# Kernel tuning notes

Hardware: AMD Instinct MI355X
Metric: run time of the kernel (lower is better)

Reference implementation:

```python
import jax, jax.numpy as jnp
import numpy as np

B, C, H, W = 8, 768, 32, 32
NH = 12
HD = C // NH
HID = 4 * C
EPS = 1e-5


def _layer_norm(x, g, b):
    mu = jnp.mean(x, axis=-1, keepdims=True)
    var = jnp.mean(jnp.square(x - mu), axis=-1, keepdims=True)
    return (x - mu) * jax.lax.rsqrt(var + EPS) * g + b


def setup_inputs() -> dict:
    key = jax.random.key(0)
    ks = jax.random.split(key, 12)
    s = 0.02
    return {
        "x": jax.random.normal(ks[0], (B, C, H, W), jnp.float32),
        "conv_w": jax.random.normal(ks[1], (C, 1, 3, 3), jnp.float32) * s,  # depthwise OIHW
        "conv_b": jnp.zeros((C,), jnp.float32),
        "ln1_g": jnp.ones((C,), jnp.float32),
        "ln1_b": jnp.zeros((C,), jnp.float32),
        "qkv_w": jax.random.normal(ks[2], (3 * C, C), jnp.float32) * s,  # no bias (qkv_bias=False)
        "proj_w": jax.random.normal(ks[3], (C, C), jnp.float32) * s,
        "proj_b": jnp.zeros((C,), jnp.float32),
        "ln2_g": jnp.ones((C,), jnp.float32),
        "ln2_b": jnp.zeros((C,), jnp.float32),
        "fc1_w": jax.random.normal(ks[4], (HID, C), jnp.float32) * s,
        "fc1_b": jnp.zeros((HID,), jnp.float32),
        "fc2_w": jax.random.normal(ks[5], (C, HID), jnp.float32) * s,
        "fc2_b": jnp.zeros((C,), jnp.float32),
    }


def reference(x, conv_w, conv_b, ln1_g, ln1_b, qkv_w, proj_w, proj_b,
              ln2_g, ln2_b, fc1_w, fc1_b, fc2_w, fc2_b):
    # depthwise 3x3 conv positional embedding, residual
    pe = jax.lax.conv_general_dilated(
        x, conv_w, window_strides=(1, 1), padding=((1, 1), (1, 1)),
        dimension_numbers=("NCHW", "OIHW", "NCHW"), feature_group_count=C)
    x = x + pe + conv_b[None, :, None, None]

    b, c, h, w = x.shape
    t = x.reshape(b, c, h * w).transpose(0, 2, 1)  # [B, N, C]

    # attention
    hn = _layer_norm(t, ln1_g, ln1_b)
    qkv = hn @ qkv_w.T  # [B, N, 3C]
    qkv = qkv.reshape(b, h * w, 3, NH, HD).transpose(2, 0, 3, 1, 4)  # [3, B, nh, N, hd]
    q, k, v = qkv[0], qkv[1], qkv[2]
    scale = HD ** -0.5
    attn = jax.nn.softmax(jnp.einsum("bhnd,bhmd->bhnm", q, k) * scale, axis=-1)
    o = jnp.einsum("bhnm,bhmd->bhnd", attn, v).transpose(0, 2, 1, 3).reshape(b, h * w, c)
    t = t + (o @ proj_w.T + proj_b)

    # MLP
    hn = _layer_norm(t, ln2_g, ln2_b)
    hid = jax.nn.gelu(hn @ fc1_w.T + fc1_b, approximate=False)
    t = t + (hid @ fc2_w.T + fc2_b)

    return t.transpose(0, 2, 1).reshape(b, c, h, w)
```

## Files before the change

kernel.cpp:

```cpp
#include <hip/hip_runtime.h>
#include <math.h>


typedef __bf16 bf16;
typedef __attribute__((ext_vector_type(8))) __bf16 bf16x8;
typedef __attribute__((ext_vector_type(4))) __bf16 bf16x4;
typedef __attribute__((ext_vector_type(4))) float f32x4;

#define B_   8
#define C_   768
#define N_   1024
#define NH_  12
#define HD_  64
#define HID_ 3072
#define NTOK   (B_ * N_)
#define NHEADS (B_ * NH_)
#define FA_C   0.1803368801111601f

__device__ __forceinline__ void gload_lds16(const void* g, void* l) {
  __builtin_amdgcn_global_load_lds(
      (__attribute__((address_space(1))) void*)(void*)g,
      (__attribute__((address_space(3))) void*)l, 16, 0, 0);
}

__device__ __forceinline__ float gelu1(float x) {
  float u = 0.7978845608028654f * x * (1.0f + 0.044715f * x * x);
  float e = __builtin_amdgcn_exp2f(u * 2.885390081777927f);
  float th = 1.0f - 2.0f * __builtin_amdgcn_rcpf(e + 1.0f);
  return 0.5f * x * (1.0f + th);
}

template <int BN, int EPI, bool REMAP>
__global__ __launch_bounds__(256) void gemm_bt(
    const bf16* __restrict__ A, const bf16* __restrict__ B, int K, int lda,
    int ldb, int ntiles, bf16* __restrict__ o0, bf16* __restrict__ o1,
    bf16* __restrict__ o2, float* __restrict__ resid,
    const float* __restrict__ bias, float* __restrict__ outp) {
  constexpr int JJ = BN / 32;
  constexpr int BCH = BN / 32;
  constexpr int STAGE_B = (128 + BN) * 64 * 2;
  constexpr int EXTRA_B = (EPI == 5) ? 64 * 132 * 4 : (EPI == 0 ? 128 * 256 : 0);
  constexpr int SMEM_B = STAGE_B > EXTRA_B ? STAGE_B : EXTRA_B;
  __shared__ __align__(16) char smemraw[SMEM_B];
  bf16* As = (bf16*)smemraw;
  bf16* Bs = As + 128 * 64;

  const int tid = threadIdx.x;
  const int wave = tid >> 6, lane = tid & 63;
  const int wm = wave & 1, wn = wave >> 1;
  const int lr = lane & 15, kq = lane >> 4;
  const int sw = lr & 7;

  int m0, n0;
  if constexpr (REMAP) {
    const int bid = blockIdx.x;
    const int g = bid & 7, s = bid >> 3;
    const int ms = s / ntiles;
    m0 = (g * 8 + ms) * 128;
    n0 = (s - ms * ntiles) * BN;
  } else {
    m0 = blockIdx.y * 128;
    n0 = blockIdx.x * BN;
  }

  f32x4 acc[4][JJ];
#pragma unroll
  for (int i = 0; i < 4; i++)
#pragma unroll
    for (int j = 0; j < JJ; j++) acc[i][j] = (f32x4){0.f, 0.f, 0.f, 0.f};

  const bf16* ap[4];
  const bf16* bp[BCH];
  {
    const bf16* Arow = A + (size_t)m0 * lda;
    const bf16* Brow = B + (size_t)n0 * ldb;
#pragma unroll
    for (int it = 0; it < 4; ++it) {
      int s = it * 256 + tid;
      int r = s >> 3, seg = (s & 7) ^ (r & 7);
      ap[it] = Arow + (size_t)r * lda + seg * 8;
    }
#pragma unroll
    for (int it = 0; it < BCH; ++it) {
      int s = it * 256 + tid;
      int r = s >> 3, seg = (s & 7) ^ (r & 7);
      bp[it] = Brow + (size_t)r * ldb + seg * 8;
    }
  }

  for (int k0 = 0; k0 < K; k0 += 64) {
#pragma unroll
    for (int it = 0; it < 4; ++it) {
      gload_lds16(ap[it], (char*)As + (it * 256 + tid) * 16);
      ap[it] += 64;
    }
#pragma unroll
    for (int it = 0; it < BCH; ++it) {
      gload_lds16(bp[it], (char*)Bs + (it * 256 + tid) * 16);
      bp[it] += 64;
    }
    __syncthreads();

#pragma unroll
    for (int h = 0; h < 2; ++h) {
      bf16x8 af[4], bfr[JJ];
      const int c = h * 4 + kq;
#pragma unroll
      for (int i = 0; i < 4; i++) {
        int row = wm * 64 + i * 16 + lr;
        af[i] = *(const bf16x8*)((char*)As + (row * 8 + (c ^ sw)) * 16);
      }
#pragma unroll
      for (int j = 0; j < JJ; j++) {
        int row = wn * (BN / 2) + j * 16 + lr;
        bfr[j] = *(const bf16x8*)((char*)Bs + (row * 8 + (c ^ sw)) * 16);
      }
#pragma unroll
      for (int i = 0; i < 4; i++)
#pragma unroll
        for (int j = 0; j < JJ; j++)
          acc[i][j] = __builtin_amdgcn_mfma_f32_16x16x32_bf16(bfr[j], af[i],
                                                              acc[i][j], 0, 0, 0);
    }
    __syncthreads();
  }

  if constexpr (EPI == 0) {
    const int b = m0 >> 10, tok0 = m0 & (N_ - 1);
    if (n0 < 2 * C_) {
      const int s = n0 >= C_ ? 1 : 0;
      bf16* dst = s ? o1 : o0;
#pragma unroll
      for (int i = 0; i < 4; i++) {
        const int m = m0 + wm * 64 + i * 16 + lr;
#pragma unroll
        for (int j = 0; j < JJ; j++) {
          const int rem = n0 - s * C_ + wn * (BN / 2) + j * 16 + kq * 4;
          const int h = rem >> 6, d = rem & 63;
          const f32x4 v = acc[i][j];
          bf16x4 pk = {(bf16)v[0], (bf16)v[1], (bf16)v[2], (bf16)v[3]};
          size_t head = (size_t)b * NH_ + h;
          *(bf16x4*)(dst + (head * N_ + (m & (N_ - 1))) * HD_ + d) = pk;
        }
      }
    } else {
      bf16* tile = (bf16*)smemraw;
#pragma unroll
      for (int i = 0; i < 4; i++) {
        const int ml = wm * 64 + i * 16 + lr;
        const int mc = ml >> 3, mo = ml & 7;
#pragma unroll
        for (int j = 0; j < JJ; j++) {
          const f32x4 v = acc[i][j];
#pragma unroll
          for (int r = 0; r < 4; r++) {
            const int nl = wn * (BN / 2) + j * 16 + kq * 4 + r;
            *(bf16*)((char*)tile + nl * 256 + ((mc ^ (nl & 15)) * 16) + mo * 2) =
                (bf16)v[r];
          }
        }
      }
      __syncthreads();
      const int nl = tid >> 1, mh = (tid & 1) * 64;
      const int vb = n0 - 2 * C_ + nl;
      const size_t head = (size_t)b * NH_ + (vb >> 6);
      bf16* dst = o2 + (head * HD_ + (vb & 63)) * N_ + tok0 + mh;
#pragma unroll
      for (int c8 = 0; c8 < 8; ++c8) {
        const int c = (mh >> 3) + c8;
        bf16x8 val = *(const bf16x8*)((char*)tile + nl * 256 +
                                      ((c ^ (nl & 15)) * 16));
        *(bf16x8*)(dst + c8 * 8) = val;
      }
    }
  } else if constexpr (EPI == 3) {
#pragma unroll
    for (int j = 0; j < JJ; j++) {
      const int n = n0 + wn * (BN / 2) + j * 16 + kq * 4;
      const f32x4 bv = *(const f32x4*)(bias + n);
#pragma unroll
      for (int i = 0; i < 4; i++) {
        const int m = m0 + wm * 64 + i * 16 + lr;
        float* rp = resid + (size_t)m * C_ + n;
        f32x4 old = *(const f32x4*)rp;
        const f32x4 v = acc[i][j];
        f32x4 nw = {old[0] + v[0] + bv[0], old[1] + v[1] + bv[1],
                    old[2] + v[2] + bv[2], old[3] + v[3] + bv[3]};
        *(f32x4*)rp = nw;
      }
    }
  } else if constexpr (EPI == 4) {
#pragma unroll
    for (int j = 0; j < JJ; j++) {
      const int n = n0 + wn * (BN / 2) + j * 16 + kq * 4;
      const f32x4 bv = *(const f32x4*)(bias + n);
#pragma unroll
      for (int i = 0; i < 4; i++) {
        const int m = m0 + wm * 64 + i * 16 + lr;
        const f32x4 v = acc[i][j];
        bf16x4 pk = {(bf16)gelu1(v[0] + bv[0]), (bf16)gelu1(v[1] + bv[1]),
                     (bf16)gelu1(v[2] + bv[2]), (bf16)gelu1(v[3] + bv[3])};
        *(bf16x4*)(o0 + (size_t)m * HID_ + n) = pk;
      }
    }
  } else if constexpr (EPI == 5) {
    float* tile = (float*)smemraw;
    const int b = m0 >> 10, tok0 = m0 & (N_ - 1);
#pragma unroll
    for (int j = 0; j < JJ; j++) {
      const int nl0 = wn * (BN / 2) + j * 16 + kq * 4;
      const int n = n0 + nl0;
      const f32x4 bv = *(const f32x4*)(bias + n);
#pragma unroll
      for (int i = 0; i < 4; i++) {
        const int ml = wm * 64 + i * 16 + lr;
        const float* rp = resid + (size_t)(m0 + ml) * C_ + n;
        f32x4 old = *(const f32x4*)rp;
        const f32x4 v = acc[i][j];
#pragma unroll
        for (int r = 0; r < 4; r++)
          tile[(nl0 + r) * 132 + ml] = old[r] + v[r] + bv[r];
      }
    }
    __syncthreads();
    const int nl = tid & 63, mc = tid >> 6;
    float* dst = outp + ((size_t)(b * C_ + n0 + nl)) * N_ + tok0 + mc * 32;
    const float* src = tile + nl * 132 + mc * 32;
#pragma unroll
    for (int q = 0; q < 8; ++q)
      *(f32x4*)(dst + q * 4) = *(const f32x4*)(src + q * 4);
  }
}

__global__ __launch_bounds__(256, 3) void flash_attn(
    const bf16* __restrict__ Qb, const bf16* __restrict__ Kb,
    const bf16* __restrict__ Vt, bf16* __restrict__ attn) {
  __shared__ __align__(16) bf16 ksm[2][64 * 64];
  __shared__ __align__(16) bf16 vsm[2][64 * 64];
  __shared__ __align__(16) bf16 psm[4][32 * 64];

  const int tid = threadIdx.x, wave = tid >> 6, lane = tid & 63;
  const int lr = lane & 15, kq = lane >> 4;
  const int head = blockIdx.y;
  const int b = head / NH_, hh = head - b * NH_;
  const int q0 = blockIdx.x * 128;
  const bf16* Qh = Qb + (size_t)head * (N_ * HD_);
  const bf16* Kh = Kb + (size_t)head * (N_ * HD_);
  const bf16* Vh = Vt + (size_t)head * (HD_ * N_);
  char* pw = (char*)&psm[wave][0];

  bf16x8 qf[2][2];
#pragma unroll
  for (int j = 0; j < 2; ++j)
#pragma unroll
    for (int kh = 0; kh < 2; ++kh)
      qf[j][kh] = *(const bf16x8*)(Qh +
                                   (size_t)(q0 + wave * 32 + j * 16 + lr) * HD_ +
                                   kh * 32 + kq * 8);

  f32x4 o[4][2];
#pragma unroll
  for (int i = 0; i < 4; i++)
#pragma unroll
    for (int j = 0; j < 2; j++) o[i][j] = (f32x4){0.f, 0.f, 0.f, 0.f};
  float mprev[2] = {-1e30f, -1e30f}, lacc[2] = {0.f, 0.f};

  auto stage = [&](int t, int bi) {
#pragma unroll
    for (int it = 0; it < 2; ++it) {
      int s = it * 256 + tid;
      int r = s >> 3, seg = (s & 7) ^ (r & 7);
      gload_lds16(Kh + (size_t)(t * 64 + r) * HD_ + seg * 8,
                  (char*)ksm[bi] + (it * 256 + wave * 64) * 16);
    }
#pragma unroll
    for (int it = 0; it < 2; ++it) {
      int s = it * 256 + tid;
      int r = s >> 3, seg = (s & 7) ^ (r & 7);
      gload_lds16(Vh + (size_t)r * N_ + t * 64 + seg * 8,
                  (char*)vsm[bi] + (it * 256 + wave * 64) * 16);
    }
  };

  stage(0, 0);

  for (int t = 0; t < 16; ++t) {
    const int bi = t & 1;
    __syncthreads();
    if (t < 15) stage(t + 1, bi ^ 1);

    f32x4 sacc[4][2];
#pragma unroll
    for (int i = 0; i < 4; ++i) {
#pragma unroll
      for (int j = 0; j < 2; ++j) sacc[i][j] = (f32x4){0.f, 0.f, 0.f, 0.f};
      int row = i * 16 + lr;
      bf16x8 kf0 = *(const bf16x8*)((char*)ksm[bi] + row * 128 +
                                    ((kq ^ (row & 7)) * 16));
      bf16x8 kf1 = *(const bf16x8*)((char*)ksm[bi] + row * 128 +
                                    (((4 + kq) ^ (row & 7)) * 16));
#pragma unroll
      for (int j = 0; j < 2; ++j) {
        sacc[i][j] = __builtin_amdgcn_mfma_f32_16x16x32_bf16(kf0, qf[j][0],
                                                             sacc[i][j], 0, 0, 0);
        sacc[i][j] = __builtin_amdgcn_mfma_f32_16x16x32_bf16(kf1, qf[j][1],
                                                             sacc[i][j], 0, 0, 0);
      }
    }

#pragma unroll
    for (int j = 0; j < 2; ++j) {
      float mx = -1e30f;
#pragma unroll
      for (int i = 0; i < 4; ++i)
#pragma unroll
        for (int r = 0; r < 4; ++r) mx = fmaxf(mx, sacc[i][j][r]);
      mx = fmaxf(mx, __shfl_xor(mx, 16));
      mx = fmaxf(mx, __shfl_xor(mx, 32));
      float mnew = fmaxf(mprev[j], mx);
      float alpha = __builtin_amdgcn_exp2f((mprev[j] - mnew) * FA_C);
      mprev[j] = mnew;
      float rs = 0.f;
      const int prow = j * 16 + lr;
#pragma unroll
      for (int i = 0; i < 4; ++i) {
        float p0 = __builtin_amdgcn_exp2f((sacc[i][j][0] - mnew) * FA_C);
        float p1 = __builtin_amdgcn_exp2f((sacc[i][j][1] - mnew) * FA_C);
        float p2 = __builtin_amdgcn_exp2f((sacc[i][j][2] - mnew) * FA_C);
        float p3 = __builtin_amdgcn_exp2f((sacc[i][j][3] - mnew) * FA_C);
        rs += (p0 + p1) + (p2 + p3);
        bf16x4 pk = {(bf16)p0, (bf16)p1, (bf16)p2, (bf16)p3};
        int c = i * 2 + (kq >> 1);
        *(bf16x4*)(pw + prow * 128 + ((c ^ (prow & 7)) * 16) + (kq & 1) * 8) = pk;
      }
      rs += __shfl_xor(rs, 16);
      rs += __shfl_xor(rs, 32);
      lacc[j] = lacc[j] * alpha + rs;
#pragma unroll
      for (int i = 0; i < 4; ++i) {
        o[i][j][0] *= alpha; o[i][j][1] *= alpha;
        o[i][j][2] *= alpha; o[i][j][3] *= alpha;
      }
    }

#pragma unroll
    for (int k0c = 0; k0c < 2; ++k0c) {
      bf16x8 pf[2];
#pragma unroll
      for (int j = 0; j < 2; ++j) {
        int prow = j * 16 + lr, c = k0c * 4 + kq;
        pf[j] = *(const bf16x8*)(pw + prow * 128 + ((c ^ (prow & 7)) * 16));
      }
#pragma unroll
      for (int i = 0; i < 4; ++i) {
        int d = i * 16 + lr, c = k0c * 4 + kq;
        bf16x8 vf = *(const bf16x8*)((char*)vsm[bi] + d * 128 +
                                     ((c ^ (d & 7)) * 16));
#pragma unroll
        for (int j = 0; j < 2; ++j)
          o[i][j] = __builtin_amdgcn_mfma_f32_16x16x32_bf16(vf, pf[j], o[i][j],
                                                            0, 0, 0);
      }
    }
  }

#pragma unroll
  for (int j = 0; j < 2; ++j) {
    float inv = 1.0f / lacc[j];
    int tok = q0 + wave * 32 + j * 16 + lr;
    bf16* op = attn + ((size_t)(b * N_ + tok)) * C_ + hh * HD_;
#pragma unroll
    for (int i = 0; i < 4; ++i) {
      bf16x4 pk = {(bf16)(o[i][j][0] * inv), (bf16)(o[i][j][1] * inv),
                   (bf16)(o[i][j][2] * inv), (bf16)(o[i][j][3] * inv)};
      *(bf16x4*)(op + i * 16 + kq * 4) = pk;
    }
  }
}

__global__ __launch_bounds__(256) void cast_all(
    const float* __restrict__ a, int na, const float* __restrict__ b, int nb,
    const float* __restrict__ c, int nc, const float* __restrict__ d,
    bf16* __restrict__ dst) {
  int i = (blockIdx.x * 256 + threadIdx.x) * 4;
  const float* src;
  int off;
  if (i < na) { src = a; off = i; }
  else if (i < na + nb) { src = b; off = i - na; }
  else if (i < na + nb + nc) { src = c; off = i - na - nb; }
  else { src = d; off = i - na - nb - nc; }
  float4 v = *(const float4*)(src + off);
  bf16x4 o = {(bf16)v.x, (bf16)v.y, (bf16)v.z, (bf16)v.w};
  *(bf16x4*)(dst + i) = o;
}

__global__ __launch_bounds__(256) void conv_pe_t(const float* __restrict__ x,
                                                 const float* __restrict__ cw,
                                                 const float* __restrict__ cb,
                                                 float* __restrict__ t0) {
  __shared__ float tile[32][33];
  const int h = blockIdx.x, ct = blockIdx.y, b = blockIdx.z;
  const int tid = threadIdx.x;
  const int w = tid & 31, cs = tid >> 5;
#pragma unroll
  for (int cc = cs; cc < 32; cc += 8) {
    int c = ct * 32 + cc;
    const float* xp = x + ((size_t)(b * C_ + c)) * 1024;
    const float* wp = cw + c * 9;
    float s = cb[c] + xp[h * 32 + w];
#pragma unroll
    for (int ky = 0; ky < 3; ++ky) {
      int hy = h + ky - 1;
      if ((unsigned)hy < 32u) {
#pragma unroll
        for (int kx = 0; kx < 3; ++kx) {
          int wx = w + kx - 1;
          if ((unsigned)wx < 32u) s += xp[hy * 32 + wx] * wp[ky * 3 + kx];
        }
      }
    }
    tile[cc][w] = s;
  }
  __syncthreads();
  const int cc = tid & 31;
#pragma unroll
  for (int wc = tid >> 5; wc < 32; wc += 8)
    t0[((size_t)(b * N_) + h * 32 + wc) * C_ + ct * 32 + cc] = tile[cc][wc];
}

__global__ __launch_bounds__(256) void ln_bf16(const float* __restrict__ t,
                                               const float* __restrict__ g,
                                               const float* __restrict__ be,
                                               bf16* __restrict__ out) {
  int row = blockIdx.x, tid = threadIdx.x;
  const float* p = t + (size_t)row * C_;
  float v0 = p[tid], v1 = p[tid + 256], v2 = p[tid + 512];
  __shared__ float rs[256], rq[256];
  rs[tid] = v0 + v1 + v2;
  rq[tid] = v0 * v0 + v1 * v1 + v2 * v2;
  __syncthreads();
  for (int off = 128; off; off >>= 1) {
    if (tid < off) {
      rs[tid] += rs[tid + off];
      rq[tid] += rq[tid + off];
    }
    __syncthreads();
  }
  float mu = rs[0] * (1.f / C_);
  float var = rq[0] * (1.f / C_) - mu * mu;
  float rstd = rsqrtf(var + 1e-5f);
  bf16* q = out + (size_t)row * C_;
  q[tid] = (bf16)((v0 - mu) * rstd * g[tid] + be[tid]);
  q[tid + 256] = (bf16)((v1 - mu) * rstd * g[tid + 256] + be[tid + 256]);
  q[tid + 512] = (bf16)((v2 - mu) * rstd * g[tid + 512] + be[tid + 512]);
}

extern "C" void kernel_launch(void* const* d_in, const int* in_sizes, int n_in,
                              void* d_out, int out_size, void* d_ws,
                              size_t ws_size, hipStream_t stream) {
  (void)in_sizes; (void)n_in; (void)out_size; (void)ws_size;
  const float* x      = (const float*)d_in[0];
  const float* conv_w = (const float*)d_in[1];
  const float* conv_b = (const float*)d_in[2];
  const float* ln1_g  = (const float*)d_in[3];
  const float* ln1_b  = (const float*)d_in[4];
  const float* qkv_w  = (const float*)d_in[5];
  const float* proj_w = (const float*)d_in[6];
  const float* proj_b = (const float*)d_in[7];
  const float* ln2_g  = (const float*)d_in[8];
  const float* ln2_b  = (const float*)d_in[9];
  const float* fc1_w  = (const float*)d_in[10];
  const float* fc1_b  = (const float*)d_in[11];
  const float* fc2_w  = (const float*)d_in[12];
  const float* fc2_b  = (const float*)d_in[13];
  float* out = (float*)d_out;

  char* w = (char*)d_ws;
  auto carve = [&](size_t bytes) {
    char* p = w;
    w += (bytes + 255) & ~(size_t)255;
    return p;
  };
  bf16* hid   = (bf16*)carve((size_t)NTOK * HID_ * 2);
  float* t0   = (float*)carve((size_t)NTOK * C_ * 4);
  bf16* lnout = (bf16*)carve((size_t)NTOK * C_ * 2);
  bf16* wq    = (bf16*)carve((size_t)3 * C_ * C_ * 2);
  bf16* wp    = (bf16*)carve((size_t)C_ * C_ * 2);
  bf16* w1    = (bf16*)carve((size_t)HID_ * C_ * 2);
  bf16* w2    = (bf16*)carve((size_t)C_ * HID_ * 2);
  bf16* Qb    = (bf16*)carve((size_t)NHEADS * N_ * HD_ * 2);
  bf16* Kb    = (bf16*)carve((size_t)NHEADS * N_ * HD_ * 2);
  bf16* Vt    = (bf16*)carve((size_t)NHEADS * HD_ * N_ * 2);
  bf16* attn  = (bf16*)carve((size_t)NTOK * C_ * 2);

  const int na = 3 * C_ * C_, nb = C_ * C_, nc = HID_ * C_, nd = C_ * HID_;
  cast_all<<<(na + nb + nc + nd) / 1024, 256, 0, stream>>>(
      qkv_w, na, proj_w, nb, fc1_w, nc, fc2_w, wq);

  conv_pe_t<<<dim3(32, C_ / 32, B_), 256, 0, stream>>>(x, conv_w, conv_b, t0);

  ln_bf16<<<NTOK, 256, 0, stream>>>(t0, ln1_g, ln1_b, lnout);
  gemm_bt<128, 0, true><<<1152, 256, 0, stream>>>(
      lnout, wq, 768, 768, 768, 18, Qb, Kb, Vt, nullptr, nullptr, nullptr);

  flash_attn<<<dim3(N_ / 128, NHEADS), 256, 0, stream>>>(Qb, Kb, Vt, attn);

  gemm_bt<64, 3, true><<<768, 256, 0, stream>>>(
      attn, wp, 768, 768, 768, 12, nullptr, nullptr, nullptr, t0, proj_b,
      nullptr);
  ln_bf16<<<NTOK, 256, 0, stream>>>(t0, ln2_g, ln2_b, lnout);
  gemm_bt<128, 4, true><<<1536, 256, 0, stream>>>(
      lnout, w1, 768, 768, 768, 24, hid, nullptr, nullptr, nullptr, fc1_b,
      nullptr);
  gemm_bt<64, 5, true><<<768, 256, 0, stream>>>(
      hid, w2, 3072, 3072, 3072, 12, nullptr, nullptr, nullptr, t0, fc2_b,
      out);
}
```

Measured before the change: 405.1 us.

## Add 256x256-tile 512-thread fc1 GEMM with quarter-staged LDS pipeline and fused GELU

Replaces the fc1 GEMM (128-wide tiles, 1536 blocks) with a new kernel using 256x256 output tiles, 8 waves and a double-buffered LDS of 128KB. Each k-step is split into four quadrant MFMA phases, with async global-to-LDS loads for the next stage issued between them and priority raised around the MFMA bursts. The goal is more data reuse per loaded byte and better overlap of loads with matrix math. In exchange it uses heavy LDS and registers, which limits occupancy to one block per CU, and launches 384 blocks, which may leave the 256 CUs unevenly loaded.

```diff
diff --git a/kernel.cpp b/kernel.cpp
--- a/kernel.cpp
+++ b/kernel.cpp
@@ -28,6 +28,238 @@
   float e = __builtin_amdgcn_exp2f(u * 2.885390081777927f);
   float th = 1.0f - 2.0f * __builtin_amdgcn_rcpf(e + 1.0f);
   return 0.5f * x * (1.0f + th);
+}
+
+#define PIPE_SYNC(N)                                              \
+  do {                                                            \
+    asm volatile("s_waitcnt vmcnt(" #N ") lgkmcnt(0)" ::: "memory"); \
+    __builtin_amdgcn_sched_barrier(0);                            \
+    __builtin_amdgcn_s_barrier();                                 \
+    __builtin_amdgcn_sched_barrier(0);                            \
+    asm volatile("" ::: "memory");                                \
+  } while (0)
+
+__global__ __launch_bounds__(512) void gemm256_gelu(
+    const bf16* __restrict__ A, const bf16* __restrict__ Bw,
+    const float* __restrict__ bias, bf16* __restrict__ outp,
+    int K, int lda, int ldb, int ntiles, int mtpx, int ldo) {
+  __shared__ __align__(16) char smem[131072];
+  const int tid = threadIdx.x;
+  const int wave = tid >> 6, lane = tid & 63;
+  const int wr = wave & 1, wc = wave >> 1;
+  const int lr = lane & 15, kq = lane >> 4;
+
+  const int bid = blockIdx.x;
+  const int g = bid & 7, s = bid >> 3;
+  const int ms = s / ntiles;
+  const int m0 = (g * mtpx + ms) * 256;
+  const int n0 = (s - ms * ntiles) * 256;
+
+  f32x4 acc[2][2][4][2];
+#pragma unroll
+  for (int qm = 0; qm < 2; ++qm)
+#pragma unroll
+    for (int qn = 0; qn < 2; ++qn)
+#pragma unroll
+      for (int i = 0; i < 4; ++i)
+#pragma unroll
+        for (int j = 0; j < 2; ++j)
+          acc[qm][qn][i][j] = (f32x4){0.f, 0.f, 0.f, 0.f};
+
+  const bf16* pa[2][2];
+  const bf16* pb[2][2];
+  int dof[2];
+#pragma unroll
+  for (int ld = 0; ld < 2; ++ld) {
+    const int sidx = ld * 512 + tid;
+    const int r = sidx >> 3, seg = (sidx & 7) ^ (r & 7);
+    pa[0][ld] = A + (size_t)(m0 + r) * lda + seg * 8;
+    pa[1][ld] = A + (size_t)(m0 + 128 + r) * lda + seg * 8;
+    pb[0][ld] = Bw + (size_t)(n0 + r) * ldb + seg * 8;
+    pb[1][ld] = Bw + (size_t)(n0 + 128 + r) * ldb + seg * 8;
+    dof[ld] = sidx * 16;
+  }
+
+  const int NT = K >> 6;
+
+  {
+    char* wb = smem;
+#pragma unroll
+    for (int ld = 0; ld < 2; ++ld) gload_lds16(pa[0][ld], wb + dof[ld]);
+#pragma unroll
+    for (int ld = 0; ld < 2; ++ld) gload_lds16(pb[0][ld], wb + 32768 + dof[ld]);
+#pragma unroll
+    for (int ld = 0; ld < 2; ++ld) gload_lds16(pa[1][ld], wb + 16384 + dof[ld]);
+#pragma unroll
+    for (int ld = 0; ld < 2; ++ld) gload_lds16(pb[1][ld], wb + 49152 + dof[ld]);
+#pragma unroll
+    for (int ld = 0; ld < 2; ++ld) {
+      pa[0][ld] += 64; pa[1][ld] += 64; pb[0][ld] += 64; pb[1][ld] += 64;
+    }
+  }
+
+  for (int t = 0; t < NT - 1; ++t) {
+    const char* rb = smem + (t & 1) * 65536;
+    char* wb = smem + ((t & 1) ^ 1) * 65536;
+    bf16x8 af0[4][2], af1[4][2], bf0[2][2], bf1[2][2];
+
+    PIPE_SYNC(4);
+#pragma unroll
+    for (int i = 0; i < 4; ++i) {
+      const int r = wr * 64 + i * 16 + lr;
+#pragma unroll
+      for (int kh = 0; kh < 2; ++kh) {
+        const int c = kh * 4 + kq;
+        af0[i][kh] = *(const bf16x8*)(rb + (r * 8 + (c ^ (r & 7))) * 16);
+      }
+    }
+#pragma unroll
+    for (int j = 0; j < 2; ++j) {
+      const int r = wc * 32 + j * 16 + lr;
+#pragma unroll
+      for (int kh = 0; kh < 2; ++kh) {
+        const int c = kh * 4 + kq;
+        bf0[j][kh] = *(const bf16x8*)(rb + 32768 + (r * 8 + (c ^ (r & 7))) * 16);
+      }
+    }
+    gload_lds16(pa[0][0], wb + dof[0]);
+    gload_lds16(pa[0][1], wb + dof[1]);
+    pa[0][0] += 64; pa[0][1] += 64;
+    __builtin_amdgcn_s_setprio(1);
+#pragma unroll
+    for (int kh = 0; kh < 2; ++kh)
+#pragma unroll
+      for (int i = 0; i < 4; ++i)
+#pragma unroll
+        for (int j = 0; j < 2; ++j)
+          acc[0][0][i][j] = __builtin_amdgcn_mfma_f32_16x16x32_bf16(
+              bf0[j][kh], af0[i][kh], acc[0][0][i][j], 0, 0, 0);
+    __builtin_amdgcn_s_setprio(0);
+
+    PIPE_SYNC(4);
+#pragma unroll
+    for (int i = 0; i < 4; ++i) {
+      const int r = wr * 64 + i * 16 + lr;
+#pragma unroll
+      for (int kh = 0; kh < 2; ++kh) {
+        const int c = kh * 4 + kq;
+        af1[i][kh] = *(const bf16x8*)(rb + 16384 + (r * 8 + (c ^ (r & 7))) * 16);
+      }
+    }
+    gload_lds16(pb[0][0], wb + 32768 + dof[0]);
+    gload_lds16(pb[0][1], wb + 32768 + dof[1]);
+    pb[0][0] += 64; pb[0][1] += 64;
+    __builtin_amdgcn_s_setprio(1);
+#pragma unroll
+    for (int kh = 0; kh < 2; ++kh)
+#pragma unroll
+      for (int i = 0; i < 4; ++i)
+#pragma unroll
+        for (int j = 0; j < 2; ++j)
+          acc[1][0][i][j] = __builtin_amdgcn_mfma_f32_16x16x32_bf16(
+              bf0[j][kh], af1[i][kh], acc[1][0][i][j], 0, 0, 0);
+    __builtin_amdgcn_s_setprio(0);
+
+    PIPE_SYNC(4);
+#pragma unroll
+    for (int j = 0; j < 2; ++j) {
+      const int r = wc * 32 + j * 16 + lr;
+#pragma unroll
+      for (int kh = 0; kh < 2; ++kh) {
+        const int c = kh * 4 + kq;
+        bf1[j][kh] = *(const bf16x8*)(rb + 49152 + (r * 8 + (c ^ (r & 7))) * 16);
+      }
+    }
+    gload_lds16(pa[1][0], wb + 16384 + dof[0]);
+    gload_lds16(pa[1][1], wb + 16384 + dof[1]);
+    pa[1][0] += 64; pa[1][1] += 64;
+    __builtin_amdgcn_s_setprio(1);
+#pragma unroll
+    for (int kh = 0; kh < 2; ++kh)
+#pragma unroll
+      for (int i = 0; i < 4; ++i)
+#pragma unroll
+        for (int j = 0; j < 2; ++j)
+          acc[0][1][i][j] = __builtin_amdgcn_mfma_f32_16x16x32_bf16(
+              bf1[j][kh], af0[i][kh], acc[0][1][i][j], 0, 0, 0);
+    __builtin_amdgcn_s_setprio(0);
+
+    PIPE_SYNC(4);
+    gload_lds16(pb[1][0], wb + 49152 + dof[0]);
+    gload_lds16(pb[1][1], wb + 49152 + dof[1]);
+    pb[1][0] += 64; pb[1][1] += 64;
+    __builtin_amdgcn_s_setprio(1);
+#pragma unroll
+    for (int kh = 0; kh < 2; ++kh)
+#pragma unroll
+      for (int i = 0; i < 4; ++i)
+#pragma unroll
+        for (int j = 0; j < 2; ++j)
+          acc[1][1][i][j] = __builtin_amdgcn_mfma_f32_16x16x32_bf16(
+              bf1[j][kh], af1[i][kh], acc[1][1][i][j], 0, 0, 0);
+    __builtin_amdgcn_s_setprio(0);
+  }
+
+  {
+    const char* rb = smem + ((NT - 1) & 1) * 65536;
+    bf16x8 af0[4][2], af1[4][2], bf0[2][2], bf1[2][2];
+    PIPE_SYNC(0);
+#pragma unroll
+    for (int i = 0; i < 4; ++i) {
+      const int r = wr * 64 + i * 16 + lr;
+#pragma unroll
+      for (int kh = 0; kh < 2; ++kh) {
+        const int c = kh * 4 + kq;
+        af0[i][kh] = *(const bf16x8*)(rb + (r * 8 + (c ^ (r & 7))) * 16);
+        af1[i][kh] = *(const bf16x8*)(rb + 16384 + (r * 8 + (c ^ (r & 7))) * 16);
+      }
+    }
+#pragma unroll
+    for (int j = 0; j < 2; ++j) {
+      const int r = wc * 32 + j * 16 + lr;
+#pragma unroll
+      for (int kh = 0; kh < 2; ++kh) {
+        const int c = kh * 4 + kq;
+        bf0[j][kh] = *(const bf16x8*)(rb + 32768 + (r * 8 + (c ^ (r & 7))) * 16);
+        bf1[j][kh] = *(const bf16x8*)(rb + 49152 + (r * 8 + (c ^ (r & 7))) * 16);
+      }
+    }
+    __builtin_amdgcn_s_setprio(1);
+#pragma unroll
+    for (int kh = 0; kh < 2; ++kh)
+#pragma unroll
+      for (int i = 0; i < 4; ++i)
+#pragma unroll
+        for (int j = 0; j < 2; ++j) {
+          acc[0][0][i][j] = __builtin_amdgcn_mfma_f32_16x16x32_bf16(
+              bf0[j][kh], af0[i][kh], acc[0][0][i][j], 0, 0, 0);
+          acc[1][0][i][j] = __builtin_amdgcn_mfma_f32_16x16x32_bf16(
+              bf0[j][kh], af1[i][kh], acc[1][0][i][j], 0, 0, 0);
+          acc[0][1][i][j] = __builtin_amdgcn_mfma_f32_16x16x32_bf16(
+              bf1[j][kh], af0[i][kh], acc[0][1][i][j], 0, 0, 0);
+          acc[1][1][i][j] = __builtin_amdgcn_mfma_f32_16x16x32_bf16(
+              bf1[j][kh], af1[i][kh], acc[1][1][i][j], 0, 0, 0);
+        }
+    __builtin_amdgcn_s_setprio(0);
+  }
+
+#pragma unroll
+  for (int qn = 0; qn < 2; ++qn)
+#pragma unroll
+    for (int j = 0; j < 2; ++j) {
+      const int n = n0 + qn * 128 + wc * 32 + j * 16 + kq * 4;
+      const f32x4 bv = *(const f32x4*)(bias + n);
+#pragma unroll
+      for (int qm = 0; qm < 2; ++qm)
+#pragma unroll
+        for (int i = 0; i < 4; ++i) {
+          const int m = m0 + qm * 128 + wr * 64 + i * 16 + lr;
+          const f32x4 v = acc[qm][qn][i][j];
+          bf16x4 pk = {(bf16)gelu1(v[0] + bv[0]), (bf16)gelu1(v[1] + bv[1]),
+                       (bf16)gelu1(v[2] + bv[2]), (bf16)gelu1(v[3] + bv[3])};
+          *(bf16x4*)(outp + (size_t)m * ldo + n) = pk;
+        }
+    }
 }
 
 template <int BN, int EPI, bool REMAP>
@@ -509,9 +741,8 @@
       attn, wp, 768, 768, 768, 12, nullptr, nullptr, nullptr, t0, proj_b,
       nullptr);
   ln_bf16<<<NTOK, 256, 0, stream>>>(t0, ln2_g, ln2_b, lnout);
-  gemm_bt<128, 4, true><<<1536, 256, 0, stream>>>(
-      lnout, w1, 768, 768, 768, 24, hid, nullptr, nullptr, nullptr, fc1_b,
-      nullptr);
+  gemm256_gelu<<<384, 512, 0, stream>>>(lnout, w1, fc1_b, hid, 768, 768, 768,
+                                        12, 4, HID_);
   gemm_bt<64, 5, true><<<768, 256, 0, stream>>>(
       hid, w2, 3072, 3072, 3072, 12, nullptr, nullptr, nullptr, t0, fc2_b,
       out);
```

New measurement: 403.2 us. About the same (-0.5%).

## Add dedicated 256x192-tile pipelined fc1 GEMM with fused GELU

Applied to the files above, without the earlier changes.

Replaces the generic 128x128 gemm_bt used for fc1 with a specialized 512-thread kernel using 256x192 output tiles, double-buffered LDS fed by direct global-to-LDS loads, and loads interleaved between MFMA phases with explicit waitcnt/barrier staging and setprio. Launch count drops to 512 blocks, one per CU-ish wave, with XCD-aware block remapping. Larger tiles raise arithmetic intensity and the staged pipeline aims to hide load latency, at the cost of higher register pressure (96 accumulator vectors) and 112KB LDS limiting occupancy to one block per CU.

```diff
diff --git a/kernel.cpp b/kernel.cpp
--- a/kernel.cpp
+++ b/kernel.cpp
@@ -28,6 +28,206 @@
   float e = __builtin_amdgcn_exp2f(u * 2.885390081777927f);
   float th = 1.0f - 2.0f * __builtin_amdgcn_rcpf(e + 1.0f);
   return 0.5f * x * (1.0f + th);
+}
+
+#define PIPE_SYNC(N)                                              \
+  do {                                                            \
+    asm volatile("s_waitcnt vmcnt(" #N ") lgkmcnt(0)" ::: "memory"); \
+    __builtin_amdgcn_sched_barrier(0);                            \
+    __builtin_amdgcn_s_barrier();                                 \
+    __builtin_amdgcn_sched_barrier(0);                            \
+    asm volatile("" ::: "memory");                                \
+  } while (0)
+
+__global__ __launch_bounds__(512) void gemm_fc1(
+    const bf16* __restrict__ A, const bf16* __restrict__ Bw,
+    const float* __restrict__ bias, bf16* __restrict__ outp,
+    int K, int lda, int ldb, int ntiles, int mtpx, int ldo) {
+  __shared__ __align__(16) char smem[114688];
+  const int tid = threadIdx.x;
+  const int wave = tid >> 6, lane = tid & 63;
+  const int wr = wave & 1, wc = wave >> 1;
+  const int lr = lane & 15, kq = lane >> 4;
+
+  const int bid = blockIdx.x;
+  const int g = bid & 7, s = bid >> 3;
+  const int ms = s / ntiles;
+  const int m0 = (g * mtpx + ms) * 256;
+  const int n0 = (s - ms * ntiles) * 192;
+
+  f32x4 acc[8][3];
+#pragma unroll
+  for (int i = 0; i < 8; ++i)
+#pragma unroll
+    for (int j = 0; j < 3; ++j) acc[i][j] = (f32x4){0.f, 0.f, 0.f, 0.f};
+
+  const bf16* pa[4];
+  const bf16* pb[3];
+  int da[4], db[3];
+#pragma unroll
+  for (int c = 0; c < 4; ++c) {
+    const int sidx = c * 512 + tid;
+    const int r = sidx >> 3, seg = (sidx & 7) ^ (r & 7);
+    pa[c] = A + (size_t)(m0 + r) * lda + seg * 8;
+    da[c] = sidx * 16;
+  }
+#pragma unroll
+  for (int c = 0; c < 3; ++c) {
+    const int sidx = c * 512 + tid;
+    const int r = sidx >> 3, seg = (sidx & 7) ^ (r & 7);
+    pb[c] = Bw + (size_t)(n0 + r) * ldb + seg * 8;
+    db[c] = 32768 + sidx * 16;
+  }
+
+  const int NT = K >> 6;
+
+  gload_lds16(pb[0], smem + db[0]);
+  gload_lds16(pb[1], smem + db[1]);
+  gload_lds16(pb[2], smem + db[2]);
+  gload_lds16(pa[0], smem + da[0]);
+  gload_lds16(pa[1], smem + da[1]);
+  gload_lds16(pa[2], smem + da[2]);
+  gload_lds16(pa[3], smem + da[3]);
+#pragma unroll
+  for (int c = 0; c < 4; ++c) pa[c] += 64;
+#pragma unroll
+  for (int c = 0; c < 3; ++c) pb[c] += 64;
+
+  for (int t = 0; t < NT - 1; ++t) {
+    const char* rb = smem + (t & 1) * 57344;
+    char* wb = smem + ((t & 1) ^ 1) * 57344;
+    bf16x8 af[4], bf0[3], bf1[3];
+
+    PIPE_SYNC(1);
+#pragma unroll
+    for (int i = 0; i < 4; ++i) {
+      const int r = wr * 128 + i * 16 + lr;
+      af[i] = *(const bf16x8*)(rb + (r * 8 + (kq ^ (r & 7))) * 16);
+    }
+#pragma unroll
+    for (int j = 0; j < 3; ++j) {
+      const int r = wc * 48 + j * 16 + lr;
+      bf0[j] = *(const bf16x8*)(rb + 32768 + (r * 8 + (kq ^ (r & 7))) * 16);
+    }
+    gload_lds16(pb[0], wb + db[0]); pb[0] += 64;
+    gload_lds16(pb[1], wb + db[1]); pb[1] += 64;
+    __builtin_amdgcn_s_setprio(1);
+#pragma unroll
+    for (int i = 0; i < 4; ++i)
+#pragma unroll
+      for (int j = 0; j < 3; ++j)
+        acc[i][j] = __builtin_amdgcn_mfma_f32_16x16x32_bf16(bf0[j], af[i],
+                                                            acc[i][j], 0, 0, 0);
+    __builtin_amdgcn_s_setprio(0);
+
+    PIPE_SYNC(2);
+#pragma unroll
+    for (int i = 0; i < 4; ++i) {
+      const int r = wr * 128 + 64 + i * 16 + lr;
+      af[i] = *(const bf16x8*)(rb + (r * 8 + (kq ^ (r & 7))) * 16);
+    }
+    gload_lds16(pb[2], wb + db[2]); pb[2] += 64;
+    gload_lds16(pa[0], wb + da[0]); pa[0] += 64;
+    __builtin_amdgcn_s_setprio(1);
+#pragma unroll
+    for (int i = 0; i < 4; ++i)
+#pragma unroll
+      for (int j = 0; j < 3; ++j)
+        acc[4 + i][j] = __builtin_amdgcn_mfma_f32_16x16x32_bf16(
+            bf0[j], af[i], acc[4 + i][j], 0, 0, 0);
+    __builtin_amdgcn_s_setprio(0);
+
+    PIPE_SYNC(4);
+#pragma unroll
+    for (int i = 0; i < 4; ++i) {
+      const int r = wr * 128 + i * 16 + lr;
+      af[i] = *(const bf16x8*)(rb + (r * 8 + ((4 + kq) ^ (r & 7))) * 16);
+    }
+#pragma unroll
+    for (int j = 0; j < 3; ++j) {
+      const int r = wc * 48 + j * 16 + lr;
+      bf1[j] = *(const bf16x8*)(rb + 32768 + (r * 8 + ((4 + kq) ^ (r & 7))) * 16);
+    }
+    gload_lds16(pa[1], wb + da[1]); pa[1] += 64;
+    gload_lds16(pa[2], wb + da[2]); pa[2] += 64;
+    __builtin_amdgcn_s_setprio(1);
+#pragma unroll
+    for (int i = 0; i < 4; ++i)
+#pragma unroll
+      for (int j = 0; j < 3; ++j)
+        acc[i][j] = __builtin_amdgcn_mfma_f32_16x16x32_bf16(bf1[j], af[i],
+                                                            acc[i][j], 0, 0, 0);
+    __builtin_amdgcn_s_setprio(0);
+
+    PIPE_SYNC(6);
+#pragma unroll
+    for (int i = 0; i < 4; ++i) {
+      const int r = wr * 128 + 64 + i * 16 + lr;
+      af[i] = *(const bf16x8*)(rb + (r * 8 + ((4 + kq) ^ (r & 7))) * 16);
+    }
+    gload_lds16(pa[3], wb + da[3]); pa[3] += 64;
+    __builtin_amdgcn_s_setprio(1);
+#pragma unroll
+    for (int i = 0; i < 4; ++i)
+#pragma unroll
+      for (int j = 0; j < 3; ++j)
+        acc[4 + i][j] = __builtin_amdgcn_mfma_f32_16x16x32_bf16(
+            bf1[j], af[i], acc[4 + i][j], 0, 0, 0);
+    __builtin_amdgcn_s_setprio(0);
+  }
+
+  {
+    const char* rb = smem + ((NT - 1) & 1) * 57344;
+    bf16x8 af[4], bf0[3], bf1[3];
+    PIPE_SYNC(0);
+#pragma unroll
+    for (int j = 0; j < 3; ++j) {
+      const int r = wc * 48 + j * 16 + lr;
+      bf0[j] = *(const bf16x8*)(rb + 32768 + (r * 8 + (kq ^ (r & 7))) * 16);
+      bf1[j] = *(const bf16x8*)(rb + 32768 + (r * 8 + ((4 + kq) ^ (r & 7))) * 16);
+    }
+    __builtin_amdgcn_s_setprio(1);
+#pragma unroll
+    for (int half = 0; half < 2; ++half) {
+#pragma unroll
+      for (int i = 0; i < 4; ++i) {
+        const int r = wr * 128 + half * 64 + i * 16 + lr;
+        af[i] = *(const bf16x8*)(rb + (r * 8 + (kq ^ (r & 7))) * 16);
+      }
+#pragma unroll
+      for (int i = 0; i < 4; ++i)
+#pragma unroll
+        for (int j = 0; j < 3; ++j)
+          acc[half * 4 + i][j] = __builtin_amdgcn_mfma_f32_16x16x32_bf16(
+              bf0[j], af[i], acc[half * 4 + i][j], 0, 0, 0);
+#pragma unroll
+      for (int i = 0; i < 4; ++i) {
+        const int r = wr * 128 + half * 64 + i * 16 + lr;
+        af[i] = *(const bf16x8*)(rb + (r * 8 + ((4 + kq) ^ (r & 7))) * 16);
+      }
+#pragma unroll
+      for (int i = 0; i < 4; ++i)
+#pragma unroll
+        for (int j = 0; j < 3; ++j)
+          acc[half * 4 + i][j] = __builtin_amdgcn_mfma_f32_16x16x32_bf16(
+              bf1[j], af[i], acc[half * 4 + i][j], 0, 0, 0);
+    }
+    __builtin_amdgcn_s_setprio(0);
+  }
+
+#pragma unroll
+  for (int j = 0; j < 3; ++j) {
+    const int n = n0 + wc * 48 + j * 16 + kq * 4;
+    const f32x4 bv = *(const f32x4*)(bias + n);
+#pragma unroll
+    for (int i = 0; i < 8; ++i) {
+      const int m = m0 + wr * 128 + i * 16 + lr;
+      const f32x4 v = acc[i][j];
+      bf16x4 pk = {(bf16)gelu1(v[0] + bv[0]), (bf16)gelu1(v[1] + bv[1]),
+                   (bf16)gelu1(v[2] + bv[2]), (bf16)gelu1(v[3] + bv[3])};
+      *(bf16x4*)(outp + (size_t)m * ldo + n) = pk;
+    }
+  }
 }
 
 template <int BN, int EPI, bool REMAP>
@@ -187,20 +387,6 @@
         f32x4 nw = {old[0] + v[0] + bv[0], old[1] + v[1] + bv[1],
                     old[2] + v[2] + bv[2], old[3] + v[3] + bv[3]};
         *(f32x4*)rp = nw;
-      }
-    }
-  } else if constexpr (EPI == 4) {
-#pragma unroll
-    for (int j = 0; j < JJ; j++) {
-      const int n = n0 + wn * (BN / 2) + j * 16 + kq * 4;
-      const f32x4 bv = *(const f32x4*)(bias + n);
-#pragma unroll
-      for (int i = 0; i < 4; i++) {
-        const int m = m0 + wm * 64 + i * 16 + lr;
-        const f32x4 v = acc[i][j];
-        bf16x4 pk = {(bf16)gelu1(v[0] + bv[0]), (bf16)gelu1(v[1] + bv[1]),
-                     (bf16)gelu1(v[2] + bv[2]), (bf16)gelu1(v[3] + bv[3])};
-        *(bf16x4*)(o0 + (size_t)m * HID_ + n) = pk;
       }
     }
   } else if constexpr (EPI == 5) {
@@ -509,9 +695,8 @@
       attn, wp, 768, 768, 768, 12, nullptr, nullptr, nullptr, t0, proj_b,
       nullptr);
   ln_bf16<<<NTOK, 256, 0, stream>>>(t0, ln2_g, ln2_b, lnout);
-  gemm_bt<128, 4, true><<<1536, 256, 0, stream>>>(
-      lnout, w1, 768, 768, 768, 24, hid, nullptr, nullptr, nullptr, fc1_b,
-      nullptr);
+  gemm_fc1<<<512, 512, 0, stream>>>(lnout, w1, fc1_b, hid, 768, 768, 768,
+                                    16, 4, HID_);
   gemm_bt<64, 5, true><<<768, 256, 0, stream>>>(
       hid, w2, 3072, 3072, 3072, 12, nullptr, nullptr, nullptr, t0, fc2_b,
       out);
```

Result: faster. 385.7 us (-4.8%).

## Add dedicated 128x96-tile MLP GEMM kernel with explicit LDS pipeline sync

Applied to the files above, without the earlier changes.

Replaces the fc1 and fc2 GEMMs with a new kernel that uses 128x96 tiles, double-buffered direct-to-LDS loads with hand-placed waitcnt/barriers and setprio around MFMA bursts. It also uses launch bounds of 2 blocks per SM. The grid is remapped to 2048 and 512 blocks to balance tile counts across the 256 CUs and reduce wave quantization. The risk is a lower arithmetic intensity per tile and tighter register pressure.

```diff
diff --git a/kernel.cpp b/kernel.cpp
--- a/kernel.cpp
+++ b/kernel.cpp
@@ -30,6 +30,177 @@
   return 0.5f * x * (1.0f + th);
 }
 
+#define PIPE_SYNC(N)                                              \
+  do {                                                            \
+    asm volatile("s_waitcnt vmcnt(" #N ") lgkmcnt(0)" ::: "memory"); \
+    __builtin_amdgcn_sched_barrier(0);                            \
+    __builtin_amdgcn_s_barrier();                                 \
+    __builtin_amdgcn_sched_barrier(0);                            \
+    asm volatile("" ::: "memory");                                \
+  } while (0)
+
+#define TILE_END_SYNC()                                           \
+  do {                                                            \
+    asm volatile("s_waitcnt lgkmcnt(0)" ::: "memory");            \
+    __builtin_amdgcn_sched_barrier(0);                            \
+    __builtin_amdgcn_s_barrier();                                 \
+    __builtin_amdgcn_sched_barrier(0);                            \
+    asm volatile("" ::: "memory");                                \
+  } while (0)
+
+template <int EPI>
+__global__ __launch_bounds__(256, 2) void gemm_mlp(
+    const bf16* __restrict__ A, const bf16* __restrict__ Bw,
+    const float* __restrict__ bias, bf16* __restrict__ o_bf,
+    const float* __restrict__ resid, float* __restrict__ o_f32,
+    int K, int lda, int ldb, int ntiles, int mtpx, int ldo) {
+  __shared__ __align__(16) char smem[57344];
+  const int tid = threadIdx.x;
+  const int wave = tid >> 6, lane = tid & 63;
+  const int wr = wave & 1, wc = wave >> 1;
+  const int lr = lane & 15, kq = lane >> 4;
+
+  const int bid = blockIdx.x;
+  const int g = bid & 7, s = bid >> 3;
+  const int ms = s / ntiles;
+  const int m0 = (g * mtpx + ms) * 128;
+  const int n0 = (s - ms * ntiles) * 96;
+
+  f32x4 acc[4][3];
+#pragma unroll
+  for (int i = 0; i < 4; ++i)
+#pragma unroll
+    for (int j = 0; j < 3; ++j) acc[i][j] = (f32x4){0.f, 0.f, 0.f, 0.f};
+
+  const bf16* pa[4];
+  const bf16* pb[3];
+  int da[4], db[3];
+#pragma unroll
+  for (int c = 0; c < 4; ++c) {
+    const int sidx = c * 256 + tid;
+    const int r = sidx >> 3, seg = (sidx & 7) ^ (r & 7);
+    pa[c] = A + (size_t)(m0 + r) * lda + seg * 8;
+    da[c] = sidx * 16;
+  }
+#pragma unroll
+  for (int c = 0; c < 3; ++c) {
+    const int sidx = c * 256 + tid;
+    const int r = sidx >> 3, seg = (sidx & 7) ^ (r & 7);
+    pb[c] = Bw + (size_t)(n0 + r) * ldb + seg * 8;
+    db[c] = 16384 + sidx * 16;
+  }
+
+  const int NT = K >> 6;
+
+  {
+    char* wb = smem;
+#pragma unroll
+    for (int c = 0; c < 4; ++c) { gload_lds16(pa[c], wb + da[c]); pa[c] += 64; }
+#pragma unroll
+    for (int c = 0; c < 3; ++c) { gload_lds16(pb[c], wb + db[c]); pb[c] += 64; }
+  }
+
+  for (int t = 0; t < NT; ++t) {
+    const char* rb = smem + (t & 1) * 28672;
+    if (t < NT - 1) {
+      char* wb = smem + ((t & 1) ^ 1) * 28672;
+#pragma unroll
+      for (int c = 0; c < 4; ++c) { gload_lds16(pa[c], wb + da[c]); pa[c] += 64; }
+#pragma unroll
+      for (int c = 0; c < 3; ++c) { gload_lds16(pb[c], wb + db[c]); pb[c] += 64; }
+      PIPE_SYNC(7);
+    } else {
+      PIPE_SYNC(0);
+    }
+
+    bf16x8 af[4], bf[3];
+#pragma unroll
+    for (int i = 0; i < 4; ++i) {
+      const int r = wr * 64 + i * 16 + lr;
+      af[i] = *(const bf16x8*)(rb + (r * 8 + (kq ^ (r & 7))) * 16);
+    }
+#pragma unroll
+    for (int j = 0; j < 3; ++j) {
+      const int r = wc * 48 + j * 16 + lr;
+      bf[j] = *(const bf16x8*)(rb + 16384 + (r * 8 + (kq ^ (r & 7))) * 16);
+    }
+    __builtin_amdgcn_s_setprio(1);
+#pragma unroll
+    for (int i = 0; i < 4; ++i)
+#pragma unroll
+      for (int j = 0; j < 3; ++j)
+        acc[i][j] = __builtin_amdgcn_mfma_f32_16x16x32_bf16(bf[j], af[i],
+                                                            acc[i][j], 0, 0, 0);
+    __builtin_amdgcn_s_setprio(0);
+#pragma unroll
+    for (int i = 0; i < 4; ++i) {
+      const int r = wr * 64 + i * 16 + lr;
+      af[i] = *(const bf16x8*)(rb + (r * 8 + ((4 + kq) ^ (r & 7))) * 16);
+    }
+#pragma unroll
+    for (int j = 0; j < 3; ++j) {
+      const int r = wc * 48 + j * 16 + lr;
+      bf[j] = *(const bf16x8*)(rb + 16384 + (r * 8 + ((4 + kq) ^ (r & 7))) * 16);
+    }
+    __builtin_amdgcn_s_setprio(1);
+#pragma unroll
+    for (int i = 0; i < 4; ++i)
+#pragma unroll
+      for (int j = 0; j < 3; ++j)
+        acc[i][j] = __builtin_amdgcn_mfma_f32_16x16x32_bf16(bf[j], af[i],
+                                                            acc[i][j], 0, 0, 0);
+    __builtin_amdgcn_s_setprio(0);
+
+    TILE_END_SYNC();
+  }
+
+  if constexpr (EPI == 0) {
+#pragma unroll
+    for (int j = 0; j < 3; ++j) {
+      const int n = n0 + wc * 48 + j * 16 + kq * 4;
+      const f32x4 bv = *(const f32x4*)(bias + n);
+#pragma unroll
+      for (int i = 0; i < 4; ++i) {
+        const int m = m0 + wr * 64 + i * 16 + lr;
+        const f32x4 v = acc[i][j];
+        bf16x4 pk = {(bf16)gelu1(v[0] + bv[0]), (bf16)gelu1(v[1] + bv[1]),
+                     (bf16)gelu1(v[2] + bv[2]), (bf16)gelu1(v[3] + bv[3])};
+        *(bf16x4*)(o_bf + (size_t)m * ldo + n) = pk;
+      }
+    }
+  } else {
+    float* tile = (float*)smem;
+    const int b = m0 >> 10, tok0 = m0 & (N_ - 1);
+#pragma unroll
+    for (int j = 0; j < 3; ++j) {
+      const int nl0 = wc * 48 + j * 16 + kq * 4;
+      const int n = n0 + nl0;
+      const f32x4 bv = *(const f32x4*)(bias + n);
+#pragma unroll
+      for (int i = 0; i < 4; ++i) {
+        const int ml = wr * 64 + i * 16 + lr;
+        const float* rp = resid + (size_t)(m0 + ml) * C_ + n;
+        f32x4 old = *(const f32x4*)rp;
+        const f32x4 v = acc[i][j];
+#pragma unroll
+        for (int r = 0; r < 4; ++r)
+          tile[(nl0 + r) * 132 + ml] = old[r] + v[r] + bv[r];
+      }
+    }
+    __syncthreads();
+    const int cl = tid >> 3, mc = tid & 7;
+#pragma unroll
+    for (int sl = 0; sl < 3; ++sl) {
+      const int rr = sl * 32 + cl;
+      float* dst = o_f32 + ((size_t)(b * C_ + n0 + rr)) * N_ + tok0 + mc * 16;
+      const float* src = tile + rr * 132 + mc * 16;
+#pragma unroll
+      for (int q = 0; q < 4; ++q)
+        *(f32x4*)(dst + q * 4) = *(const f32x4*)(src + q * 4);
+    }
+  }
+}
+
 template <int BN, int EPI, bool REMAP>
 __global__ __launch_bounds__(256) void gemm_bt(
     const bf16* __restrict__ A, const bf16* __restrict__ B, int K, int lda,
@@ -39,7 +210,7 @@
   constexpr int JJ = BN / 32;
   constexpr int BCH = BN / 32;
   constexpr int STAGE_B = (128 + BN) * 64 * 2;
-  constexpr int EXTRA_B = (EPI == 5) ? 64 * 132 * 4 : (EPI == 0 ? 128 * 256 : 0);
+  constexpr int EXTRA_B = (EPI == 0 ? 128 * 256 : 0);
   constexpr int SMEM_B = STAGE_B > EXTRA_B ? STAGE_B : EXTRA_B;
   __shared__ __align__(16) char smemraw[SMEM_B];
   bf16* As = (bf16*)smemraw;
@@ -189,46 +360,6 @@
         *(f32x4*)rp = nw;
       }
     }
-  } else if constexpr (EPI == 4) {
-#pragma unroll
-    for (int j = 0; j < JJ; j++) {
-      const int n = n0 + wn * (BN / 2) + j * 16 + kq * 4;
-      const f32x4 bv = *(const f32x4*)(bias + n);
-#pragma unroll
-      for (int i = 0; i < 4; i++) {
-        const int m = m0 + wm * 64 + i * 16 + lr;
-        const f32x4 v = acc[i][j];
-        bf16x4 pk = {(bf16)gelu1(v[0] + bv[0]), (bf16)gelu1(v[1] + bv[1]),
-                     (bf16)gelu1(v[2] + bv[2]), (bf16)gelu1(v[3] + bv[3])};
-        *(bf16x4*)(o0 + (size_t)m * HID_ + n) = pk;
-      }
-    }
-  } else if constexpr (EPI == 5) {
-    float* tile = (float*)smemraw;
-    const int b = m0 >> 10, tok0 = m0 & (N_ - 1);
-#pragma unroll
-    for (int j = 0; j < JJ; j++) {
-      const int nl0 = wn * (BN / 2) + j * 16 + kq * 4;
-      const int n = n0 + nl0;
-      const f32x4 bv = *(const f32x4*)(bias + n);
-#pragma unroll
-      for (int i = 0; i < 4; i++) {
-        const int ml = wm * 64 + i * 16 + lr;
-        const float* rp = resid + (size_t)(m0 + ml) * C_ + n;
-        f32x4 old = *(const f32x4*)rp;
-        const f32x4 v = acc[i][j];
-#pragma unroll
-        for (int r = 0; r < 4; r++)
-          tile[(nl0 + r) * 132 + ml] = old[r] + v[r] + bv[r];
-      }
-    }
-    __syncthreads();
-    const int nl = tid & 63, mc = tid >> 6;
-    float* dst = outp + ((size_t)(b * C_ + n0 + nl)) * N_ + tok0 + mc * 32;
-    const float* src = tile + nl * 132 + mc * 32;
-#pragma unroll
-    for (int q = 0; q < 8; ++q)
-      *(f32x4*)(dst + q * 4) = *(const f32x4*)(src + q * 4);
   }
 }
 
@@ -509,10 +640,8 @@
       attn, wp, 768, 768, 768, 12, nullptr, nullptr, nullptr, t0, proj_b,
       nullptr);
   ln_bf16<<<NTOK, 256, 0, stream>>>(t0, ln2_g, ln2_b, lnout);
-  gemm_bt<128, 4, true><<<1536, 256, 0, stream>>>(
-      lnout, w1, 768, 768, 768, 24, hid, nullptr, nullptr, nullptr, fc1_b,
-      nullptr);
-  gemm_bt<64, 5, true><<<768, 256, 0, stream>>>(
-      hid, w2, 3072, 3072, 3072, 12, nullptr, nullptr, nullptr, t0, fc2_b,
-      out);
-}
+  gemm_mlp<0><<<2048, 256, 0, stream>>>(lnout, w1, fc1_b, hid, nullptr,
+                                        nullptr, 768, 768, 768, 32, 8, HID_);
+  gemm_mlp<1><<<512, 256, 0, stream>>>(hid, w2, fc2_b, nullptr, t0, out,
+                                       3072, 3072, 3072, 8, 8, 0);
+}
```

Result: faster. 391.9 us (-3.2%).
